# Optimization experiments

Hardware: AMD Instinct MI355X
Metric: run time of the kernel (lower is better)

## Reference

```python
import jax, jax.numpy as jnp
import numpy as np

B, S, H = 4, 2048, 1024
NH = 16
D = H // NH
SCALE = 1.0 / np.sqrt(D).astype(np.float32)


def setup_inputs() -> dict:
    key = jax.random.key(0)
    ks = jax.random.split(key, 5)
    s = 1.0 / np.sqrt(H).astype(np.float32)  # ~ torch Linear init scale
    return {
        "x": jax.random.normal(ks[0], (B, S, H), jnp.float32),
        "Wq": jax.random.normal(ks[1], (H, H), jnp.float32) * s,
        "bq": jnp.zeros((H,), jnp.float32),
        "Wk": jax.random.normal(ks[2], (H, H), jnp.float32) * s,
        "bk": jnp.zeros((H,), jnp.float32),
        "Wv": jax.random.normal(ks[3], (H, H), jnp.float32) * s,
        "bv": jnp.zeros((H,), jnp.float32),
        "Wo": jax.random.normal(ks[4], (H, H), jnp.float32) * s,
        "bo": jnp.zeros((H,), jnp.float32),
    }


def reference(x, Wq, bq, Wk, bk, Wv, bv, Wo, bo):
    b, s, h = x.shape
    # qkv projections, split into heads: [b, nh, s, d]
    q = (x @ Wq.T + bq).reshape(b, s, NH, D).transpose(0, 2, 1, 3)
    k = (x @ Wk.T + bk).reshape(b, s, NH, D).transpose(0, 2, 1, 3)
    v = (x @ Wv.T + bv).reshape(b, s, NH, D).transpose(0, 2, 1, 3)
    att = jnp.einsum("bhqd,bhkd->bhqk", q, k) * SCALE
    att = jax.nn.softmax(att, axis=-1)  # stable max-subtract softmax
    # dropout(p=0.5) is identity in eval mode
    out = jnp.einsum("bhqk,bhkd->bhqd", att, v)
    out = out.transpose(0, 2, 1, 3).reshape(b, s, h)
    return out @ Wo.T + bo
```

## Files before the change

kernel.cpp:

```cpp
#include <hip/hip_runtime.h>
#include <hip/hip_bf16.h>
#include <stdint.h>
#include <math.h>

#define NB 4
#define NS 2048
#define NHID 1024
#define NHEAD 16
#define ND 64
#define NM (NB * NS)

typedef unsigned short u16;
typedef __attribute__((ext_vector_type(8))) short bf16x8;
typedef __attribute__((ext_vector_type(4))) float f32x4;

#define SC2F 0.18033688011112042f


__device__ __forceinline__ u16 f2bf(float f) {
  union { float f; unsigned u; } v; v.f = f;
  unsigned u = v.u;
  return (u16)((u + 0x7FFFu + ((u >> 16) & 1u)) >> 16);
}

__device__ __forceinline__ void gload_lds16(const u16* g, u16* l) {
  __builtin_amdgcn_global_load_lds(
      (const __attribute__((address_space(1))) void*)g,
      (__attribute__((address_space(3))) void*)l, 16, 0, 0);
}

__device__ __forceinline__ f32x4 mfma16(bf16x8 a, bf16x8 b, f32x4 c) {
  return __builtin_amdgcn_mfma_f32_16x16x32_bf16(a, b, c, 0, 0, 0);
}

__device__ __forceinline__ unsigned cvtpk(float lo, float hi) {
  unsigned d;
  asm("v_cvt_pk_bf16_f32 %0, %1, %2" : "=v"(d) : "v"(lo), "v"(hi));
  return d;
}


__global__ __launch_bounds__(256) void convert_f32_bf16(
    const float* __restrict__ x, const float* __restrict__ wq,
    const float* __restrict__ wk, const float* __restrict__ wv,
    const float* __restrict__ wo,
    u16* __restrict__ xb, u16* __restrict__ wqb, u16* __restrict__ wkb,
    u16* __restrict__ wvb, u16* __restrict__ wob) {
  const float* src; u16* dst; int n;
  switch (blockIdx.y) {
    case 0:  src = x;  dst = xb;  n = NM * NHID;   break;
    case 1:  src = wq; dst = wqb; n = NHID * NHID; break;
    case 2:  src = wk; dst = wkb; n = NHID * NHID; break;
    case 3:  src = wv; dst = wvb; n = NHID * NHID; break;
    default: src = wo; dst = wob; n = NHID * NHID; break;
  }
  int stride = gridDim.x * blockDim.x * 4;
  for (int i = (blockIdx.x * blockDim.x + threadIdx.x) * 4; i < n; i += stride) {
    float4 v = *reinterpret_cast<const float4*>(src + i);
    ushort4 o;
    o.x = f2bf(v.x); o.y = f2bf(v.y); o.z = f2bf(v.z); o.w = f2bf(v.w);
    *reinterpret_cast<ushort4*>(dst + i) = o;
  }
}


#define GNKT 32

__device__ __forceinline__ void gemm256_mainloop(
    const u16* __restrict__ A, const u16* __restrict__ Bw,
    int bm, int bn, u16 (*lds)[12288], f32x4 (&acc)[4][4]) {
  const int t = threadIdx.x;
  const int w = t >> 6, l = t & 63;
  const int lr = l & 15, kh = l >> 4;
  const int wm = w >> 1, wn = w & 1;

#pragma unroll
  for (int mi = 0; mi < 4; ++mi)
#pragma unroll
    for (int ni = 0; ni < 4; ++ni) acc[mi][ni] = (f32x4){0.f, 0.f, 0.f, 0.f};

  auto stage = [&](int kt, int buf) {
    const int k0 = kt * 32;
#pragma unroll
    for (int it = 0; it < 2; ++it) {
      int idx = it * 512 + t;
      int row = idx >> 2, c = idx & 3;
      gload_lds16(A + (size_t)(bm + row) * NHID + k0 + c * 8,
                  lds[buf] + (size_t)(it * 512 + w * 64) * 8);
    }
    {
      int row = t >> 2, c = t & 3;
      gload_lds16(Bw + (size_t)(bn + row) * NHID + k0 + c * 8,
                  lds[buf] + 8192 + (size_t)(w * 64) * 8);
    }
  };

  stage(0, 0);
  stage(1, 1);

  for (int kt = 0; kt < GNKT; ++kt) {
    const int buf = kt % 3;
    if (kt < GNKT - 1) asm volatile("s_waitcnt vmcnt(3)" ::: "memory");
    else               asm volatile("s_waitcnt vmcnt(0)" ::: "memory");
    __builtin_amdgcn_s_barrier();
    if (kt + 2 < GNKT) stage(kt + 2, (kt + 2) % 3);

    const u16* Ab = lds[buf];
    const u16* Bb = lds[buf] + 8192;
    bf16x8 af[4], bfr[4];
#pragma unroll
    for (int mi = 0; mi < 4; ++mi)
      af[mi] = *(const bf16x8*)&Ab[(wm * 64 + mi * 16 + lr) * 32 + kh * 8];
#pragma unroll
    for (int ni = 0; ni < 4; ++ni)
      bfr[ni] = *(const bf16x8*)&Bb[(wn * 64 + ni * 16 + lr) * 32 + kh * 8];
    __builtin_amdgcn_s_setprio(1);
#pragma unroll
    for (int mi = 0; mi < 4; ++mi)
#pragma unroll
      for (int ni = 0; ni < 4; ++ni)
        acc[mi][ni] = mfma16(af[mi], bfr[ni], acc[mi][ni]);
    __builtin_amdgcn_s_setprio(0);
  }
}


__global__ __launch_bounds__(512, 4) void gemm_qkv(
    const u16* __restrict__ xb,
    const u16* __restrict__ wqb, const u16* __restrict__ wkb, const u16* __restrict__ wvb,
    const float* __restrict__ bq, const float* __restrict__ bk, const float* __restrict__ bv,
    u16* __restrict__ Qo, u16* __restrict__ Ko, u16* __restrict__ Vo) {
  __shared__ __align__(16) u16 lds[3][12288];
  const int which = blockIdx.z;
  const u16* Bw = (which == 0) ? wqb : (which == 1) ? wkb : wvb;
  const float* bias = (which == 0) ? bq : (which == 1) ? bk : bv;
  u16* outp = (which == 0) ? Qo : (which == 1) ? Ko : Vo;
  const int bm = blockIdx.x * 256, bn = blockIdx.y * 128;

  f32x4 acc[4][4];
  gemm256_mainloop(xb, Bw, bm, bn, lds, acc);

  const int t = threadIdx.x, w = t >> 6, l = t & 63, lr = l & 15, kh = l >> 4;
  const int wm = w >> 1, wn = w & 1;
#pragma unroll
  for (int mi = 0; mi < 4; ++mi)
#pragma unroll
    for (int ni = 0; ni < 4; ++ni)
#pragma unroll
      for (int r = 0; r < 4; ++r) {
        int m = bm + wm * 64 + mi * 16 + kh * 4 + r;
        int n = bn + wn * 64 + ni * 16 + lr;
        float v = acc[mi][ni][r] + bias[n];
        if (which == 0) v *= SC2F;
        int b = m >> 11, s = m & (NS - 1), h = n >> 6, d = n & (ND - 1);
        size_t addr;
        if (which < 2) {
          addr = (((size_t)(b * NHEAD + h)) * NS + s) * ND + d;
        } else {
          int sp = (s & ~31) | (((s >> 2) & 3) * 8 + ((s >> 4) & 1) * 4 + (s & 3));
          addr = (((size_t)(b * NHEAD + h)) * ND + d) * NS + sp;
        }
        outp[addr] = f2bf(v);
      }
}


__global__ __launch_bounds__(256, 2) void attn_kernel(
    const u16* __restrict__ Q, const u16* __restrict__ K,
    const u16* __restrict__ Vt, u16* __restrict__ AO) {
  __shared__ __align__(16) u16 Ks[2][64 * 64];
  __shared__ __align__(16) u16 Vs[2][64 * 64];

  const int t = threadIdx.x, w = t >> 6, l = t & 63;
  const int lr = l & 15, g = l >> 4;
  const int bh = blockIdx.y;
  const int q0 = blockIdx.x * 256;

  const u16* Qh = Q  + (size_t)bh * NS * ND;
  const u16* Kh = K  + (size_t)bh * NS * ND;
  const u16* Vh = Vt + (size_t)bh * NS * ND;

  bf16x8 qf[4][2];
#pragma unroll
  for (int mi = 0; mi < 4; ++mi)
#pragma unroll
    for (int ks = 0; ks < 2; ++ks)
      qf[mi][ks] = *(const bf16x8*)(Qh + (size_t)(q0 + w * 64 + mi * 16 + lr) * ND + ks * 32 + g * 8);

  bf16x8 ones;
#pragma unroll
  for (int i = 0; i < 8; ++i) ones[i] = (short)0x3F80;

  auto stage_kv = [&](int kt, int b) {
#pragma unroll
    for (int j = 0; j < 2; ++j) {
      int idx = j * 256 + t;
      int row = idx >> 3, sch = (idx & 7) ^ (row & 7);
      gload_lds16(Kh + (size_t)(kt + row) * ND + sch * 8, Ks[b] + (size_t)(j * 256 + w * 64) * 8);
      gload_lds16(Vh + (size_t)row * NS + kt + sch * 8,   Vs[b] + (size_t)(j * 256 + w * 64) * 8);
    }
  };

  stage_kv(0, 0);

  f32x4 o[4][4];
  f32x4 acc_l[4];
#pragma unroll
  for (int mi = 0; mi < 4; ++mi) {
#pragma unroll
    for (int ni = 0; ni < 4; ++ni) o[mi][ni] = (f32x4){0.f, 0.f, 0.f, 0.f};
    acc_l[mi] = (f32x4){0.f, 0.f, 0.f, 0.f};
  }

  const int nt = NS / 64;
  for (int ti = 0; ti < nt; ++ti) {
    const int b = ti & 1;
    __syncthreads();
    if (ti + 1 < nt) stage_kv((ti + 1) * 64, b ^ 1);

    f32x4 s[4][4];
#pragma unroll
    for (int mi = 0; mi < 4; ++mi)
#pragma unroll
      for (int ni = 0; ni < 4; ++ni) s[mi][ni] = (f32x4){0.f, 0.f, 0.f, 0.f};
    __builtin_amdgcn_s_setprio(1);
#pragma unroll
    for (int ks = 0; ks < 2; ++ks)
#pragma unroll
      for (int ni = 0; ni < 4; ++ni) {
        bf16x8 kf = *(const bf16x8*)&Ks[b][(ni * 16 + lr) * 64 + ((ks * 4 + g) ^ (lr & 7)) * 8];
#pragma unroll
        for (int mi = 0; mi < 4; ++mi)
          s[mi][ni] = mfma16(kf, qf[mi][ks], s[mi][ni]);
      }
    __builtin_amdgcn_s_setprio(0);

#pragma unroll
    for (int mi = 0; mi < 4; ++mi)
#pragma unroll
      for (int ni = 0; ni < 4; ++ni)
#pragma unroll
        for (int r = 0; r < 4; ++r)
          s[mi][ni][r] = __builtin_amdgcn_exp2f(s[mi][ni][r]);

    __builtin_amdgcn_s_setprio(1);
#pragma unroll
    for (int ks = 0; ks < 2; ++ks) {
      union { bf16x8 v; unsigned u[4]; } pa[4];
#pragma unroll
      for (int mi = 0; mi < 4; ++mi) {
        pa[mi].u[0] = cvtpk(s[mi][2 * ks][0], s[mi][2 * ks][1]);
        pa[mi].u[1] = cvtpk(s[mi][2 * ks][2], s[mi][2 * ks][3]);
        pa[mi].u[2] = cvtpk(s[mi][2 * ks + 1][0], s[mi][2 * ks + 1][1]);
        pa[mi].u[3] = cvtpk(s[mi][2 * ks + 1][2], s[mi][2 * ks + 1][3]);
      }
#pragma unroll
      for (int ni = 0; ni < 4; ++ni) {
        bf16x8 vf = *(const bf16x8*)&Vs[b][(ni * 16 + lr) * 64 + ((ks * 4 + g) ^ (lr & 7)) * 8];
#pragma unroll
        for (int mi = 0; mi < 4; ++mi)
          o[mi][ni] = mfma16(pa[mi].v, vf, o[mi][ni]);
      }
#pragma unroll
      for (int mi = 0; mi < 4; ++mi)
        acc_l[mi] = mfma16(pa[mi].v, ones, acc_l[mi]);
    }
    __builtin_amdgcn_s_setprio(0);
  }

  const int bb = bh >> 4, h = bh & (NHEAD - 1);
#pragma unroll
  for (int mi = 0; mi < 4; ++mi) {
    f32x4 inv;
#pragma unroll
    for (int r = 0; r < 4; ++r) inv[r] = 1.0f / acc_l[mi][r];
#pragma unroll
    for (int ni = 0; ni < 4; ++ni)
#pragma unroll
      for (int r = 0; r < 4; ++r) {
        int srow = q0 + w * 64 + mi * 16 + g * 4 + r;
        int col  = h * ND + ni * 16 + lr;
        AO[(size_t)(bb * NS + srow) * NHID + col] = f2bf(o[mi][ni][r] * inv[r]);
      }
  }
}


__global__ __launch_bounds__(512, 4) void gemm_out(
    const u16* __restrict__ AO, const u16* __restrict__ wob,
    const float* __restrict__ bo, float* __restrict__ out) {
  __shared__ __align__(16) u16 lds[3][12288];
  const int bm = blockIdx.x * 256, bn = blockIdx.y * 128;

  f32x4 acc[4][4];
  gemm256_mainloop(AO, wob, bm, bn, lds, acc);

  const int t = threadIdx.x, w = t >> 6, l = t & 63, lr = l & 15, kh = l >> 4;
  const int wm = w >> 1, wn = w & 1;
#pragma unroll
  for (int mi = 0; mi < 4; ++mi)
#pragma unroll
    for (int ni = 0; ni < 4; ++ni)
#pragma unroll
      for (int r = 0; r < 4; ++r) {
        int m = bm + wm * 64 + mi * 16 + kh * 4 + r;
        int n = bn + wn * 64 + ni * 16 + lr;
        out[(size_t)m * NHID + n] = acc[mi][ni][r] + bo[n];
      }
}


extern "C" void kernel_launch(void* const* d_in, const int* in_sizes, int n_in,
                              void* d_out, int out_size, void* d_ws, size_t ws_size,
                              hipStream_t stream) {
  const float* x  = (const float*)d_in[0];
  const float* Wq = (const float*)d_in[1];
  const float* bq = (const float*)d_in[2];
  const float* Wk = (const float*)d_in[3];
  const float* bk = (const float*)d_in[4];
  const float* Wv = (const float*)d_in[5];
  const float* bv = (const float*)d_in[6];
  const float* Wo = (const float*)d_in[7];
  const float* bo = (const float*)d_in[8];
  float* out = (float*)d_out;

  char* ws = (char*)d_ws;
  u16* xb  = (u16*)(ws + 0);
  u16* wqb = (u16*)(ws + 16777216);
  u16* wkb = (u16*)(ws + 18874368);
  u16* wvb = (u16*)(ws + 20971520);
  u16* wob = (u16*)(ws + 23068672);
  u16* Qb  = (u16*)(ws + 25165824);
  u16* Kb  = (u16*)(ws + 41943040);
  u16* Vtb = (u16*)(ws + 58720256);
  u16* AOb = (u16*)(ws + 75497472);

  convert_f32_bf16<<<dim3(512, 5), 256, 0, stream>>>(x, Wq, Wk, Wv, Wo, xb, wqb, wkb, wvb, wob);
  gemm_qkv<<<dim3(32, 8, 3), 512, 0, stream>>>(xb, wqb, wkb, wvb, bq, bk, bv, Qb, Kb, Vtb);
  attn_kernel<<<dim3(8, 64), 256, 0, stream>>>(Qb, Kb, Vtb, AOb);
  gemm_out<<<dim3(32, 8), 512, 0, stream>>>(AOb, wob, bo, out);
}
```

Measured before the change: 173.8 us.

## Remap GEMM blocks for XCD locality and software-pipeline QK/exp in attention

Both GEMM kernels now launch a 1D grid and remap block IDs so that consecutive tiles sharing A/B panels land on the same XCD (stride-8 round-robin), aiming for better L2 reuse. The attention inner loop preloads all K fragments into registers, then interleaves QK^T MFMAs for one row group with exp2 and bf16 packing of an earlier group, so transcendental work can overlap matrix-core work. This raises register pressure (kfr plus pa buffers), which could reduce occupancy or cause spills.

```diff
diff --git a/kernel.cpp b/kernel.cpp
--- a/kernel.cpp
+++ b/kernel.cpp
@@ -131,11 +131,15 @@
     const float* __restrict__ bq, const float* __restrict__ bk, const float* __restrict__ bv,
     u16* __restrict__ Qo, u16* __restrict__ Ko, u16* __restrict__ Vo) {
   __shared__ __align__(16) u16 lds[3][12288];
-  const int which = blockIdx.z;
+  const int phys = blockIdx.x;
+  const int lin = (phys & 7) * 96 + (phys >> 3);
+  const int which = lin >> 8;
+  const int rem = lin & 255;
+  const int bm = (rem & 31) * 256;
+  const int bn = (rem >> 5) * 128;
   const u16* Bw = (which == 0) ? wqb : (which == 1) ? wkb : wvb;
   const float* bias = (which == 0) ? bq : (which == 1) ? bk : bv;
   u16* outp = (which == 0) ? Qo : (which == 1) ? Ko : Vo;
-  const int bm = blockIdx.x * 256, bn = blockIdx.y * 128;
 
   f32x4 acc[4][4];
   gemm256_mainloop(xb, Bw, bm, bn, lds, acc);
@@ -218,52 +222,58 @@
     __syncthreads();
     if (ti + 1 < nt) stage_kv((ti + 1) * 64, b ^ 1);
 
+    bf16x8 kfr[2][4];
+#pragma unroll
+    for (int ks = 0; ks < 2; ++ks)
+#pragma unroll
+      for (int ni = 0; ni < 4; ++ni)
+        kfr[ks][ni] = *(const bf16x8*)&Ks[b][(ni * 16 + lr) * 64 + ((ks * 4 + g) ^ (lr & 7)) * 8];
+
     f32x4 s[4][4];
-#pragma unroll
-    for (int mi = 0; mi < 4; ++mi)
-#pragma unroll
-      for (int ni = 0; ni < 4; ++ni) s[mi][ni] = (f32x4){0.f, 0.f, 0.f, 0.f};
+    union pau { bf16x8 v; unsigned u[4]; };
+    pau pa[4][2];
     __builtin_amdgcn_s_setprio(1);
 #pragma unroll
-    for (int ks = 0; ks < 2; ++ks)
-#pragma unroll
-      for (int ni = 0; ni < 4; ++ni) {
-        bf16x8 kf = *(const bf16x8*)&Ks[b][(ni * 16 + lr) * 64 + ((ks * 4 + g) ^ (lr & 7)) * 8];
-#pragma unroll
-        for (int mi = 0; mi < 4; ++mi)
-          s[mi][ni] = mfma16(kf, qf[mi][ks], s[mi][ni]);
-      }
-    __builtin_amdgcn_s_setprio(0);
-
-#pragma unroll
-    for (int mi = 0; mi < 4; ++mi)
-#pragma unroll
-      for (int ni = 0; ni < 4; ++ni)
-#pragma unroll
-        for (int r = 0; r < 4; ++r)
-          s[mi][ni][r] = __builtin_amdgcn_exp2f(s[mi][ni][r]);
-
-    __builtin_amdgcn_s_setprio(1);
+    for (int p = 0; p < 6; ++p) {
+      if (p < 4) {
+        const int mi = p;
+#pragma unroll
+        for (int ni = 0; ni < 4; ++ni) s[mi][ni] = (f32x4){0.f, 0.f, 0.f, 0.f};
+#pragma unroll
+        for (int ks = 0; ks < 2; ++ks)
+#pragma unroll
+          for (int ni = 0; ni < 4; ++ni)
+            s[mi][ni] = mfma16(kfr[ks][ni], qf[mi][ks], s[mi][ni]);
+      }
+      if (p >= 2) {
+        const int mi = p - 2;
+#pragma unroll
+        for (int ni = 0; ni < 4; ++ni)
+#pragma unroll
+          for (int r = 0; r < 4; ++r)
+            s[mi][ni][r] = __builtin_amdgcn_exp2f(s[mi][ni][r]);
+#pragma unroll
+        for (int ks = 0; ks < 2; ++ks) {
+          pa[mi][ks].u[0] = cvtpk(s[mi][2 * ks][0], s[mi][2 * ks][1]);
+          pa[mi][ks].u[1] = cvtpk(s[mi][2 * ks][2], s[mi][2 * ks][3]);
+          pa[mi][ks].u[2] = cvtpk(s[mi][2 * ks + 1][0], s[mi][2 * ks + 1][1]);
+          pa[mi][ks].u[3] = cvtpk(s[mi][2 * ks + 1][2], s[mi][2 * ks + 1][3]);
+        }
+      }
+    }
+
 #pragma unroll
     for (int ks = 0; ks < 2; ++ks) {
-      union { bf16x8 v; unsigned u[4]; } pa[4];
-#pragma unroll
-      for (int mi = 0; mi < 4; ++mi) {
-        pa[mi].u[0] = cvtpk(s[mi][2 * ks][0], s[mi][2 * ks][1]);
-        pa[mi].u[1] = cvtpk(s[mi][2 * ks][2], s[mi][2 * ks][3]);
-        pa[mi].u[2] = cvtpk(s[mi][2 * ks + 1][0], s[mi][2 * ks + 1][1]);
-        pa[mi].u[3] = cvtpk(s[mi][2 * ks + 1][2], s[mi][2 * ks + 1][3]);
-      }
 #pragma unroll
       for (int ni = 0; ni < 4; ++ni) {
         bf16x8 vf = *(const bf16x8*)&Vs[b][(ni * 16 + lr) * 64 + ((ks * 4 + g) ^ (lr & 7)) * 8];
 #pragma unroll
         for (int mi = 0; mi < 4; ++mi)
-          o[mi][ni] = mfma16(pa[mi].v, vf, o[mi][ni]);
+          o[mi][ni] = mfma16(pa[mi][ks].v, vf, o[mi][ni]);
       }
 #pragma unroll
       for (int mi = 0; mi < 4; ++mi)
-        acc_l[mi] = mfma16(pa[mi].v, ones, acc_l[mi]);
+        acc_l[mi] = mfma16(pa[mi][ks].v, ones, acc_l[mi]);
     }
     __builtin_amdgcn_s_setprio(0);
   }
@@ -290,7 +300,10 @@
     const u16* __restrict__ AO, const u16* __restrict__ wob,
     const float* __restrict__ bo, float* __restrict__ out) {
   __shared__ __align__(16) u16 lds[3][12288];
-  const int bm = blockIdx.x * 256, bn = blockIdx.y * 128;
+  const int phys = blockIdx.x;
+  const int lin = (phys & 7) * 32 + (phys >> 3);
+  const int bm = (lin & 31) * 256;
+  const int bn = (lin >> 5) * 128;
 
   f32x4 acc[4][4];
   gemm256_mainloop(AO, wob, bm, bn, lds, acc);
@@ -336,7 +349,7 @@
   u16* AOb = (u16*)(ws + 75497472);
 
   convert_f32_bf16<<<dim3(512, 5), 256, 0, stream>>>(x, Wq, Wk, Wv, Wo, xb, wqb, wkb, wvb, wob);
-  gemm_qkv<<<dim3(32, 8, 3), 512, 0, stream>>>(xb, wqb, wkb, wvb, bq, bk, bv, Qb, Kb, Vtb);
+  gemm_qkv<<<768, 512, 0, stream>>>(xb, wqb, wkb, wvb, bq, bk, bv, Qb, Kb, Vtb);
   attn_kernel<<<dim3(8, 64), 256, 0, stream>>>(Qb, Kb, Vtb, AOb);
-  gemm_out<<<dim3(32, 8), 512, 0, stream>>>(AOb, wob, bo, out);
-}
+  gemm_out<<<256, 512, 0, stream>>>(AOb, wob, bo, out);
+}
```

Measured after the change: 203.1 us. 16.8% more time.
